# Optimization experiments

Measured on AMD Instinct MI355X. Metric: run time of the kernel, lower is better.

The kernel has to match this reference:

```python
import jax, jax.numpy as jnp
import numpy as np

B, N, H = 512, 100, 768
I = 2 * H  # intermediate_dim default = hidden_dim * 2
NUM_ANS = 16
MAX_ANS = 15
LN_EPS = 1e-5


def setup_inputs() -> dict:
    key = jax.random.key(0)
    ks = jax.random.split(key, 7)
    s = 0.02
    return {
        "v_emb": jax.random.normal(ks[0], (B, N, H), dtype=jnp.float32),
        "W1": jax.random.normal(ks[1], (H, I), dtype=jnp.float32) * s,
        "b1": jax.random.normal(ks[2], (I,), dtype=jnp.float32) * s,
        "gamma": jnp.ones((I,), dtype=jnp.float32),
        "beta": jnp.zeros((I,), dtype=jnp.float32),
        "W2": jax.random.normal(ks[3], (I, 1), dtype=jnp.float32) * s,
        "b2": jax.random.normal(ks[4], (1,), dtype=jnp.float32) * s,
    }


def reference(v_emb, W1, b1, gamma, beta, W2, b2):
    # Linear -> GELU (exact/erf, torch nn.GELU default) -> LayerNorm -> Linear
    h = jnp.einsum("bnh,hi->bni", v_emb, W1) + b1            # [B,N,I]
    h = jax.nn.gelu(h, approximate=False)
    mu = jnp.mean(h, axis=-1, keepdims=True)
    var = jnp.mean(jnp.square(h - mu), axis=-1, keepdims=True)
    h = (h - mu) * jax.lax.rsqrt(var + LN_EPS) * gamma + beta
    scores = jnp.einsum("bni,io->bno", h, W2) + b2           # [B,N,1]
    scores = jax.nn.sigmoid(scores)                           # sigmoid=True branch
    pred = jnp.sum(scores, axis=1)                            # [B,1]
    # pred_to_logits: vectorized round + clamp + one-hot scatter
    # str(int(round(p))) in {'0'..'15'} -> that id; negative -> 0; overflow -> max_ans
    aid = jnp.clip(jnp.round(pred[:, 0]).astype(jnp.int32), 0, MAX_ANS)
    logits = jax.nn.one_hot(aid, NUM_ANS, dtype=scores.dtype)  # [B,16]
    # original returns dict: scores, final_attention_map (==scores), pred, logits
    return scores, pred, logits
```

## Files before the change

kernel.cpp:

```cpp
#include <hip/hip_runtime.h>
#include <hip/hip_bf16.h>
#include <cstdint>
#include <cstddef>

#define BB   512
#define NN   100
#define HH   768
#define II   1536
#define MM   (BB*NN)

typedef __bf16 bf16;
typedef __bf16 bf16x8 __attribute__((ext_vector_type(8)));
typedef float  f32x4  __attribute__((ext_vector_type(4)));
typedef float  f32x4v __attribute__((ext_vector_type(4)));

__device__ __forceinline__ void gld_lds16(const bf16* g, bf16* l) {
    __builtin_amdgcn_global_load_lds(
        (const __attribute__((address_space(1))) void*)g,
        (__attribute__((address_space(3))) void*)l, 16, 0, 0);
}

template <int CTRL>
__device__ __forceinline__ float ror_add(float x) {
    int y = __builtin_amdgcn_update_dpp(0, __float_as_int(x), CTRL, 0xF, 0xF, false);
    return x + __int_as_float(y);
}
__device__ __forceinline__ float red16(float x) {
    x = ror_add<0x121>(x);
    x = ror_add<0x122>(x);
    x = ror_add<0x124>(x);
    x = ror_add<0x128>(x);
    return x;
}

__device__ __forceinline__ float fast_gelu(float x) {
    const float ax = fabsf(x) * 0.70710678118654752f;
    const float t  = __builtin_amdgcn_rcpf(fmaf(0.3275911f, ax, 1.0f));
    float p = fmaf(1.061405429f, t, -1.453152027f);
    p = fmaf(p, t, 1.421413741f);
    p = fmaf(p, t, -0.284496736f);
    p = fmaf(p, t, 0.254829592f);
    p = p * t;
    const float e    = __expf(-ax * ax);
    const float erfa = fmaf(-p, e, 1.0f);
    const float erfx = copysignf(erfa, x);
    return 0.5f * x * (1.0f + erfx);
}

__global__ __launch_bounds__(256) void prep_conv(
    const float* __restrict__ v, const float* __restrict__ W1,
    const float* __restrict__ gamma, const float* __restrict__ beta,
    const float* __restrict__ W2, const float* __restrict__ b2,
    bf16* __restrict__ Av, bf16* __restrict__ Wp,
    float* __restrict__ gw, float* __restrict__ scal)
{
    const int bid = blockIdx.x;
    if (bid < 6400) {
        const int r = threadIdx.x >> 5;
        const int j = threadIdx.x & 31;
        const size_t m = (size_t)bid * 8 + r;
        const float* src = v + m * HH;
        bf16* dst = Av + m * HH;
        const int x = (int)(m & 7);
        #pragma unroll
        for (int u = 0; u < 3; ++u) {
            const int p = u * 32 + j;
            const int g = (p & ~7) | ((p & 7) ^ x);
            f32x4v a = __builtin_nontemporal_load((const f32x4v*)(src + g * 8));
            f32x4v b = __builtin_nontemporal_load((const f32x4v*)(src + g * 8 + 4));
            bf16x8 o = { (bf16)a[0],(bf16)a[1],(bf16)a[2],(bf16)a[3],
                         (bf16)b[0],(bf16)b[1],(bf16)b[2],(bf16)b[3] };
            *(bf16x8*)(dst + p * 8) = o;
        }
    } else if (bid < 6976) {
        const int t = (bid - 6400) * 256 + threadIdx.x;
        const int n = t % II;
        const int g = t / II;
        const int p = (g & ~7) | ((g & 7) ^ (n & 7));
        bf16x8 o;
        #pragma unroll
        for (int i = 0; i < 8; ++i)
            o[i] = (bf16)W1[(size_t)(g * 8 + i) * II + n];
        *(bf16x8*)&Wp[(size_t)n * HH + p * 8] = o;
    } else if (bid == 6976) {
        for (int j = threadIdx.x; j < II; j += 256)
            gw[j] = gamma[j] * W2[j];
    } else {
        float s1 = 0.f, s2 = 0.f;
        for (int j = threadIdx.x; j < II; j += 256) {
            float w2 = W2[j];
            s1 += gamma[j] * w2;
            s2 += beta[j]  * w2;
        }
        #pragma unroll
        for (int off = 32; off; off >>= 1) {
            s1 += __shfl_down(s1, off, 64);
            s2 += __shfl_down(s2, off, 64);
        }
        __shared__ float a1[4], a2[4];
        int lane = threadIdx.x & 63, w = threadIdx.x >> 6;
        if (lane == 0) { a1[w] = s1; a2[w] = s2; }
        __syncthreads();
        if (threadIdx.x == 0) {
            scal[0] = a1[0] + a1[1] + a1[2] + a1[3];
            scal[1] = a2[0] + a2[1] + a2[2] + a2[3] + b2[0];
        }
    }
}

__global__ __launch_bounds__(256) void gemm_part(
    const bf16* __restrict__ Av, const bf16* __restrict__ Wp,
    const float* __restrict__ b1, const float* __restrict__ gw,
    float* __restrict__ part)
{
    __shared__ bf16  As[128 * 64];
    __shared__ bf16  Bs[128 * 64];
    __shared__ float sred[2][128][3];

    const int tid  = threadIdx.x;
    const int lin  = (blockIdx.x & 7) * 600 + (blockIdx.x >> 3);
    const int mb   = lin / 12;
    const int nb   = lin % 12;
    const int lane = tid & 63;
    const int w    = tid >> 6;
    const int wm   = w >> 1;
    const int wn   = w & 1;
    const int m15  = lane & 15;
    const int q    = lane >> 4;
    const int row0 = mb * 128;

    const int srow = tid >> 3;
    const int sc   = tid & 7;
    const bf16* aP = Av + (size_t)(row0     + srow) * HH + sc * 8;
    const bf16* bP = Wp + (size_t)(nb * 128 + srow) * HH + sc * 8;
    bf16* asD = As + tid * 8;
    bf16* bsD = Bs + tid * 8;

    f32x4 acc[4][4] = {};

    for (int kt = 0; kt < 12; ++kt) {
        const int ko = kt * 64;
        #pragma unroll
        for (int i = 0; i < 4; ++i)
            gld_lds16(aP + (size_t)(32 * i) * HH + ko, asD + i * 2048);
        #pragma unroll
        for (int i = 0; i < 4; ++i)
            gld_lds16(bP + (size_t)(32 * i) * HH + ko, bsD + i * 2048);
        asm volatile("s_waitcnt vmcnt(0)" ::: "memory");
        __syncthreads();

        #pragma unroll
        for (int kb = 0; kb < 2; ++kb) {
            const int xsel = ((kb * 4 + q) ^ (m15 & 7)) * 8;
            bf16x8 af[4];
            #pragma unroll
            for (int mt = 0; mt < 4; ++mt)
                af[mt] = *(const bf16x8*)&As[(wm*64 + mt*16 + m15)*64 + xsel];
            #pragma unroll
            for (int nt = 0; nt < 4; ++nt) {
                bf16x8 bfr = *(const bf16x8*)&Bs[(wn*64 + nt*16 + m15)*64 + xsel];
                #pragma unroll
                for (int mt = 0; mt < 4; ++mt)
                    acc[mt][nt] = __builtin_amdgcn_mfma_f32_16x16x32_bf16(
                        af[mt], bfr, acc[mt][nt], 0, 0, 0);
            }
        }
        __syncthreads();
    }

    float bv[4], gv[4];
    #pragma unroll
    for (int nt = 0; nt < 4; ++nt) {
        const int col = nb*128 + wn*64 + nt*16 + m15;
        bv[nt] = b1[col];
        gv[nt] = gw[col];
    }

    #pragma unroll
    for (int mt = 0; mt < 4; ++mt) {
        #pragma unroll
        for (int r = 0; r < 4; ++r) {
            float x0 = 0.f, x1 = 0.f, x2 = 0.f;
            #pragma unroll
            for (int nt = 0; nt < 4; ++nt) {
                float g = fast_gelu(acc[mt][nt][r] + bv[nt]);
                x0 += g; x1 += g * g; x2 += g * gv[nt];
            }
            x0 = red16(x0); x1 = red16(x1); x2 = red16(x2);
            if (m15 == 0) {
                const int rl = wm*64 + mt*16 + q*4 + r;
                sred[wn][rl][0] = x0;
                sred[wn][rl][1] = x1;
                sred[wn][rl][2] = x2;
            }
        }
    }
    __syncthreads();

    if (tid < 128) {
        const size_t rg = (size_t)row0 + tid;
        #pragma unroll
        for (int s = 0; s < 3; ++s)
            part[(size_t)s * 12 * MM + (size_t)nb * MM + rg]
                = sred[0][tid][s] + sred[1][tid][s];
    }
}

__global__ __launch_bounds__(128) void score_pred(
    const float* __restrict__ part, const float* __restrict__ scal,
    float* __restrict__ o_scores, float* __restrict__ o_pred,
    float* __restrict__ o_logits)
{
    const int b = blockIdx.x, t = threadIdx.x;
    float s = 0.f;
    if (t < NN) {
        const size_t row = (size_t)b * NN + t;
        float Sh = 0.f, Shh = 0.f, Shg = 0.f;
        #pragma unroll
        for (int j = 0; j < 12; ++j) {
            Sh  += part[(size_t)0*12*MM + (size_t)j*MM + row];
            Shh += part[(size_t)1*12*MM + (size_t)j*MM + row];
            Shg += part[(size_t)2*12*MM + (size_t)j*MM + row];
        }
        const float mu   = Sh * (1.0f / II);
        const float var  = Shh * (1.0f / II) - mu * mu;
        const float rstd = rsqrtf(var + 1e-5f);
        const float z    = rstd * (Shg - mu * scal[0]) + scal[1];
        s = 1.0f / (1.0f + __expf(-z));
        o_scores[row] = s;
    }
    float v = s;
    #pragma unroll
    for (int off = 32; off; off >>= 1) v += __shfl_down(v, off, 64);
    __shared__ float ssum[2];
    const int lane = t & 63, w = t >> 6;
    if (lane == 0) ssum[w] = v;
    __syncthreads();
    const float p = ssum[0] + ssum[1];
    if (t == 0) o_pred[b] = p;
    if (t < 16) {
        int aid = (int)rintf(p);
        aid = aid < 0 ? 0 : (aid > 15 ? 15 : aid);
        o_logits[b * 16 + t] = (t == aid) ? 1.0f : 0.0f;
    }
}

extern "C" void kernel_launch(void* const* d_in, const int* in_sizes, int n_in,
                              void* d_out, int out_size, void* d_ws, size_t ws_size,
                              hipStream_t stream)
{
    const float* v_emb = (const float*)d_in[0];
    const float* W1    = (const float*)d_in[1];
    const float* b1    = (const float*)d_in[2];
    const float* gamma = (const float*)d_in[3];
    const float* beta  = (const float*)d_in[4];
    const float* W2    = (const float*)d_in[5];
    const float* b2    = (const float*)d_in[6];

    char* ws = (char*)d_ws;
    size_t off = 0;
    bf16*  Wp   = (bf16*)(ws + off);  off += (size_t)II * HH * 2;
    float* gw   = (float*)(ws + off); off += (size_t)II * 4;
    float* scal = (float*)(ws + off); off += 256;
    float* part = (float*)(ws + off); off += (size_t)MM * 36 * 4;
    bf16*  Av   = (bf16*)(ws + off);  off += (size_t)MM * HH * 2;

    float* out       = (float*)d_out;
    float* o_scores  = out;
    float* o_pred    = out + MM;
    float* o_logits  = out + MM + BB;

    hipLaunchKernelGGL(prep_conv, dim3(6978), dim3(256), 0, stream,
                       v_emb, W1, gamma, beta, W2, b2, Av, Wp, gw, scal);
    hipLaunchKernelGGL(gemm_part, dim3((MM / 128) * 12), dim3(256),
                       0, stream, Av, Wp, b1, gw, part);
    hipLaunchKernelGGL(score_pred, dim3(BB), dim3(128), 0, stream,
                       part, scal, o_scores, o_pred, o_logits);
}
```

Measured before the change: 393.6 us.

## Fuse fp32-to-bf16 activation conversion into GEMM A-tile loads

Drops the separate pass that converted v_emb to a swizzled bf16 copy. The GEMM now streams fp32 activations straight into LDS through global_load_lds with an XOR swizzle, and converts them to bf16 when it builds the MFMA fragments. This removes one full read of the fp32 input plus a write and re-read of the bf16 copy. In exchange, every A tile is re-read from global memory 12 times (once per N block) at twice the byte width, LDS use for A doubles, and conversion work is added to the inner loop.

After: 451.9 us. +14.8%, slower.

```diff
diff --git a/kernel.cpp b/kernel.cpp
--- a/kernel.cpp
+++ b/kernel.cpp
@@ -12,9 +12,8 @@
 typedef __bf16 bf16;
 typedef __bf16 bf16x8 __attribute__((ext_vector_type(8)));
 typedef float  f32x4  __attribute__((ext_vector_type(4)));
-typedef float  f32x4v __attribute__((ext_vector_type(4)));
-
-__device__ __forceinline__ void gld_lds16(const bf16* g, bf16* l) {
+
+__device__ __forceinline__ void gld_lds16(const void* g, void* l) {
     __builtin_amdgcn_global_load_lds(
         (const __attribute__((address_space(1))) void*)g,
         (__attribute__((address_space(3))) void*)l, 16, 0, 0);
@@ -47,33 +46,15 @@
     return 0.5f * x * (1.0f + erfx);
 }
 
-__global__ __launch_bounds__(256) void prep_conv(
-    const float* __restrict__ v, const float* __restrict__ W1,
-    const float* __restrict__ gamma, const float* __restrict__ beta,
-    const float* __restrict__ W2, const float* __restrict__ b2,
-    bf16* __restrict__ Av, bf16* __restrict__ Wp,
-    float* __restrict__ gw, float* __restrict__ scal)
+__global__ __launch_bounds__(256) void prep_w(
+    const float* __restrict__ W1, const float* __restrict__ gamma,
+    const float* __restrict__ beta, const float* __restrict__ W2,
+    const float* __restrict__ b2,
+    bf16* __restrict__ Wp, float* __restrict__ gw, float* __restrict__ scal)
 {
     const int bid = blockIdx.x;
-    if (bid < 6400) {
-        const int r = threadIdx.x >> 5;
-        const int j = threadIdx.x & 31;
-        const size_t m = (size_t)bid * 8 + r;
-        const float* src = v + m * HH;
-        bf16* dst = Av + m * HH;
-        const int x = (int)(m & 7);
-        #pragma unroll
-        for (int u = 0; u < 3; ++u) {
-            const int p = u * 32 + j;
-            const int g = (p & ~7) | ((p & 7) ^ x);
-            f32x4v a = __builtin_nontemporal_load((const f32x4v*)(src + g * 8));
-            f32x4v b = __builtin_nontemporal_load((const f32x4v*)(src + g * 8 + 4));
-            bf16x8 o = { (bf16)a[0],(bf16)a[1],(bf16)a[2],(bf16)a[3],
-                         (bf16)b[0],(bf16)b[1],(bf16)b[2],(bf16)b[3] };
-            *(bf16x8*)(dst + p * 8) = o;
-        }
-    } else if (bid < 6976) {
-        const int t = (bid - 6400) * 256 + threadIdx.x;
+    if (bid < 576) {
+        const int t = bid * 256 + threadIdx.x;
         const int n = t % II;
         const int g = t / II;
         const int p = (g & ~7) | ((g & 7) ^ (n & 7));
@@ -82,7 +63,7 @@
         for (int i = 0; i < 8; ++i)
             o[i] = (bf16)W1[(size_t)(g * 8 + i) * II + n];
         *(bf16x8*)&Wp[(size_t)n * HH + p * 8] = o;
-    } else if (bid == 6976) {
+    } else if (bid == 576) {
         for (int j = threadIdx.x; j < II; j += 256)
             gw[j] = gamma[j] * W2[j];
     } else {
@@ -109,11 +90,11 @@
 }
 
 __global__ __launch_bounds__(256) void gemm_part(
-    const bf16* __restrict__ Av, const bf16* __restrict__ Wp,
+    const float* __restrict__ Af, const bf16* __restrict__ Wp,
     const float* __restrict__ b1, const float* __restrict__ gw,
     float* __restrict__ part)
 {
-    __shared__ bf16  As[128 * 64];
+    __shared__ float AsF[128 * 64];
     __shared__ bf16  Bs[128 * 64];
     __shared__ float sred[2][128][3];
 
@@ -129,36 +110,48 @@
     const int q    = lane >> 4;
     const int row0 = mb * 128;
 
+    const int arow = tid >> 4;
+    const int ac   = tid & 15;
+    const int acs  = (ac & 8) | ((ac & 7) ^ (arow & 7));
+    const float* aPf = Af + (size_t)(row0 + arow) * HH + acs * 4;
+    float* asD = AsF + tid * 4;
+
     const int srow = tid >> 3;
     const int sc   = tid & 7;
-    const bf16* aP = Av + (size_t)(row0     + srow) * HH + sc * 8;
     const bf16* bP = Wp + (size_t)(nb * 128 + srow) * HH + sc * 8;
-    bf16* asD = As + tid * 8;
     bf16* bsD = Bs + tid * 8;
 
     f32x4 acc[4][4] = {};
 
     for (int kt = 0; kt < 12; ++kt) {
-        const int ko = kt * 64;
+        const float* ak = aPf + kt * 64;
+        const bf16*  bk = bP  + kt * 64;
+        #pragma unroll
+        for (int i = 0; i < 8; ++i)
+            gld_lds16(ak + (size_t)(16 * i) * HH, asD + i * 1024);
         #pragma unroll
         for (int i = 0; i < 4; ++i)
-            gld_lds16(aP + (size_t)(32 * i) * HH + ko, asD + i * 2048);
-        #pragma unroll
-        for (int i = 0; i < 4; ++i)
-            gld_lds16(bP + (size_t)(32 * i) * HH + ko, bsD + i * 2048);
+            gld_lds16(bk + (size_t)(32 * i) * HH, bsD + i * 2048);
         asm volatile("s_waitcnt vmcnt(0)" ::: "memory");
         __syncthreads();
 
         #pragma unroll
         for (int kb = 0; kb < 2; ++kb) {
-            const int xsel = ((kb * 4 + q) ^ (m15 & 7)) * 8;
+            const int xb = ((kb * 4 + q) ^ (m15 & 7)) * 8;
+            const int p0 = (2 * q) ^ (m15 & 7);
             bf16x8 af[4];
             #pragma unroll
-            for (int mt = 0; mt < 4; ++mt)
-                af[mt] = *(const bf16x8*)&As[(wm*64 + mt*16 + m15)*64 + xsel];
+            for (int mt = 0; mt < 4; ++mt) {
+                const int r = wm*64 + mt*16 + m15;
+                const f32x4* Arow = (const f32x4*)&AsF[r*64 + kb*32];
+                f32x4 lo = Arow[p0];
+                f32x4 hi = Arow[p0 ^ 1];
+                af[mt] = (bf16x8){ (bf16)lo[0],(bf16)lo[1],(bf16)lo[2],(bf16)lo[3],
+                                   (bf16)hi[0],(bf16)hi[1],(bf16)hi[2],(bf16)hi[3] };
+            }
             #pragma unroll
             for (int nt = 0; nt < 4; ++nt) {
-                bf16x8 bfr = *(const bf16x8*)&Bs[(wn*64 + nt*16 + m15)*64 + xsel];
+                bf16x8 bfr = *(const bf16x8*)&Bs[(wn*64 + nt*16 + m15)*64 + xb];
                 #pragma unroll
                 for (int mt = 0; mt < 4; ++mt)
                     acc[mt][nt] = __builtin_amdgcn_mfma_f32_16x16x32_bf16(
@@ -263,17 +256,16 @@
     float* gw   = (float*)(ws + off); off += (size_t)II * 4;
     float* scal = (float*)(ws + off); off += 256;
     float* part = (float*)(ws + off); off += (size_t)MM * 36 * 4;
-    bf16*  Av   = (bf16*)(ws + off);  off += (size_t)MM * HH * 2;
 
     float* out       = (float*)d_out;
     float* o_scores  = out;
     float* o_pred    = out + MM;
     float* o_logits  = out + MM + BB;
 
-    hipLaunchKernelGGL(prep_conv, dim3(6978), dim3(256), 0, stream,
-                       v_emb, W1, gamma, beta, W2, b2, Av, Wp, gw, scal);
+    hipLaunchKernelGGL(prep_w, dim3(578), dim3(256), 0, stream,
+                       W1, gamma, beta, W2, b2, Wp, gw, scal);
     hipLaunchKernelGGL(gemm_part, dim3((MM / 128) * 12), dim3(256),
-                       0, stream, Av, Wp, b1, gw, part);
+                       0, stream, v_emb, Wp, b1, gw, part);
     hipLaunchKernelGGL(score_pred, dim3(BB), dim3(128), 0, stream,
                        part, scal, o_scores, o_pred, o_logits);
 }
```
